# Optimization experiments

Measured on AMD Instinct MI355X. Metric: run time of the kernel, lower is better.

Reference implementation:

```python
import jax, jax.numpy as jnp
import numpy as np

N_ROWS = 1048576   # total clips
D = 128            # embedding dim
N_SEG = 2048       # number of videos (segments)
SEG_LEN = N_ROWS // N_SEG


def setup_inputs() -> dict:
    key = jax.random.key(0)
    k1, k2 = jax.random.split(key)
    clip_remap = jax.random.normal(k1, (N_ROWS, D), dtype=jnp.float32)
    clip_emb = jax.random.normal(k2, (N_ROWS, D), dtype=jnp.float32)
    # ragged segment lengths; constant here, must sum to N_ROWS
    num_list = jnp.full((N_SEG,), SEG_LEN, dtype=jnp.int32)
    return {"clip_remap": clip_remap, "clip_emb": clip_emb, "num_list": num_list}


def reference(clip_remap, clip_emb, num_list):
    n = clip_remap.shape[0]
    diff = clip_remap - clip_emb                       # [N, D]
    score_sub = jnp.sqrt(jnp.sum(diff * diff, axis=1))  # [N] per-row L2 distance
    # segment id per row from ragged lengths (static total length -> jit ok)
    seg_ids = jnp.repeat(jnp.arange(num_list.shape[0]), num_list,
                         total_repeat_length=n)        # [N]
    denom = num_list[seg_ids].astype(score_sub.dtype)  # [N] segment length per row
    return jnp.sum(score_sub / denom)                  # scalar loss
```

## Files before the change

### kernel.cpp

```cpp
#include <hip/hip_runtime.h>
#include <math.h>

typedef float v4f __attribute__((ext_vector_type(4)));

__global__ __launch_bounds__(256) void prep_kernel(const int* __restrict__ num_list,
                                                   int n_seg,
                                                   float* __restrict__ out,
                                                   int* __restrict__ seg_start) {
    __shared__ int s_sum[256];
    const int tid = threadIdx.x;
    const int C  = (n_seg + 255) >> 8;
    const int lo = tid * C;
    const int hi = (lo + C < n_seg) ? (lo + C) : n_seg;

    int sum = 0;
    for (int i = lo; i < hi; ++i) sum += num_list[i];
    s_sum[tid] = sum;
    __syncthreads();

    for (int off = 1; off < 256; off <<= 1) {
        int v   = s_sum[tid];
        int add = (tid >= off) ? s_sum[tid - off] : 0;
        __syncthreads();
        s_sum[tid] = v + add;
        __syncthreads();
    }

    int excl = (tid == 0) ? 0 : s_sum[tid - 1];
    for (int i = lo; i < hi; ++i) {
        seg_start[i] = excl;
        excl += num_list[i];
    }
    if (tid == 0) out[0] = 0.0f;
}

__global__ __launch_bounds__(256) void euclid_loss_kernel(
    const float* __restrict__ remap,
    const float* __restrict__ emb,
    const int*   __restrict__ num_list,
    const int*   __restrict__ seg_start_arr,
    float*       __restrict__ out)
{
    const int seg  = blockIdx.x;
    const int tid  = threadIdx.x;
    const int wid  = tid >> 6;
    const int lane = tid & 63;
    const int sub  = lane >> 5;
    const int l32  = lane & 31;

    const int seg_start = seg_start_arr[seg];
    const int seg_len   = num_list[seg];

    const v4f* __restrict__ pa = (const v4f*)remap;
    const v4f* __restrict__ pb = (const v4f*)emb;

    float acc = 0.0f;
    int r = wid * 2 + sub;

    for (; r + 8 < seg_len; r += 16) {
        const long long row0 = (long long)(seg_start + r);
        const long long row1 = row0 + 8;
        const v4f a0 = __builtin_nontemporal_load(pa + row0 * 32 + l32);
        const v4f b0 = __builtin_nontemporal_load(pb + row0 * 32 + l32);
        const v4f a1 = __builtin_nontemporal_load(pa + row1 * 32 + l32);
        const v4f b1 = __builtin_nontemporal_load(pb + row1 * 32 + l32);
        const v4f d0 = a0 - b0;
        const v4f d1 = a1 - b1;
        float s0 = d0[0]*d0[0] + d0[1]*d0[1] + d0[2]*d0[2] + d0[3]*d0[3];
        float s1 = d1[0]*d1[0] + d1[1]*d1[1] + d1[2]*d1[2] + d1[3]*d1[3];
        #pragma unroll
        for (int m = 1; m <= 16; m <<= 1) s0 += __shfl_xor(s0, m, 64);
        #pragma unroll
        for (int m = 1; m <= 16; m <<= 1) s1 += __shfl_xor(s1, m, 64);
        if (l32 == 0) acc += sqrtf(s0) + sqrtf(s1);
    }
    for (; r < seg_len; r += 8) {
        const long long row = (long long)(seg_start + r);
        const v4f a = __builtin_nontemporal_load(pa + row * 32 + l32);
        const v4f b = __builtin_nontemporal_load(pb + row * 32 + l32);
        const v4f d = a - b;
        float s = d[0]*d[0] + d[1]*d[1] + d[2]*d[2] + d[3]*d[3];
        #pragma unroll
        for (int m = 1; m <= 16; m <<= 1) s += __shfl_xor(s, m, 64);
        if (l32 == 0) acc += sqrtf(s);
    }

    #pragma unroll
    for (int off = 32; off >= 1; off >>= 1) acc += __shfl_down(acc, off, 64);
    __shared__ float s_acc[4];
    if (lane == 0) s_acc[wid] = acc;
    __syncthreads();
    if (tid == 0) {
        atomicAdd(out, (s_acc[0] + s_acc[1] + s_acc[2] + s_acc[3]) / (float)seg_len);
    }
}

extern "C" void kernel_launch(void* const* d_in, const int* in_sizes, int n_in,
                              void* d_out, int out_size, void* d_ws, size_t ws_size,
                              hipStream_t stream) {
    const float* remap    = (const float*)d_in[0];
    const float* emb      = (const float*)d_in[1];
    const int*   num_list = (const int*)d_in[2];
    float*       out      = (float*)d_out;
    int*         seg_start = (int*)d_ws;

    const int n_seg = in_sizes[2];

    prep_kernel<<<1, 256, 0, stream>>>(num_list, n_seg, out, seg_start);
    euclid_loss_kernel<<<n_seg, 256, 0, stream>>>(remap, emb, num_list, seg_start, out);
}
```

Before: 176.9 us.

## Compute segment offsets per block, unroll row loop, replace atomics with final reduce

Drops the single-block prefix-scan kernel: each block now sums num_list over the preceding segments itself to get its start row. Per-segment results are written to workspace and summed by a small final reduce kernel instead of atomically added. This gives a deterministic sum and removes the serial scan ahead of the main kernel. The main loop is unrolled to four rows per half-wave to keep more loads in flight. The cost is redundant prefix reads, which grow with the segment index, and an extra launch after the main kernel.

After: 166.5 us. -5.9%, faster.

```diff
diff --git a/kernel.cpp b/kernel.cpp
--- a/kernel.cpp
+++ b/kernel.cpp
@@ -3,43 +3,11 @@
 
 typedef float v4f __attribute__((ext_vector_type(4)));
 
-__global__ __launch_bounds__(256) void prep_kernel(const int* __restrict__ num_list,
-                                                   int n_seg,
-                                                   float* __restrict__ out,
-                                                   int* __restrict__ seg_start) {
-    __shared__ int s_sum[256];
-    const int tid = threadIdx.x;
-    const int C  = (n_seg + 255) >> 8;
-    const int lo = tid * C;
-    const int hi = (lo + C < n_seg) ? (lo + C) : n_seg;
-
-    int sum = 0;
-    for (int i = lo; i < hi; ++i) sum += num_list[i];
-    s_sum[tid] = sum;
-    __syncthreads();
-
-    for (int off = 1; off < 256; off <<= 1) {
-        int v   = s_sum[tid];
-        int add = (tid >= off) ? s_sum[tid - off] : 0;
-        __syncthreads();
-        s_sum[tid] = v + add;
-        __syncthreads();
-    }
-
-    int excl = (tid == 0) ? 0 : s_sum[tid - 1];
-    for (int i = lo; i < hi; ++i) {
-        seg_start[i] = excl;
-        excl += num_list[i];
-    }
-    if (tid == 0) out[0] = 0.0f;
-}
-
 __global__ __launch_bounds__(256) void euclid_loss_kernel(
     const float* __restrict__ remap,
     const float* __restrict__ emb,
     const int*   __restrict__ num_list,
-    const int*   __restrict__ seg_start_arr,
-    float*       __restrict__ out)
+    float*       __restrict__ ws)
 {
     const int seg  = blockIdx.x;
     const int tid  = threadIdx.x;
@@ -48,7 +16,19 @@
     const int sub  = lane >> 5;
     const int l32  = lane & 31;
 
-    const int seg_start = seg_start_arr[seg];
+    __shared__ int   s_red[4];
+    __shared__ int   s_start;
+    __shared__ float s_acc[4];
+
+    int partial = 0;
+    for (int i = tid; i < seg; i += 256) partial += num_list[i];
+    #pragma unroll
+    for (int off = 32; off >= 1; off >>= 1) partial += __shfl_down(partial, off, 64);
+    if (lane == 0) s_red[wid] = partial;
+    __syncthreads();
+    if (tid == 0) s_start = s_red[0] + s_red[1] + s_red[2] + s_red[3];
+    __syncthreads();
+    const int seg_start = s_start;
     const int seg_len   = num_list[seg];
 
     const v4f* __restrict__ pa = (const v4f*)remap;
@@ -57,22 +37,32 @@
     float acc = 0.0f;
     int r = wid * 2 + sub;
 
-    for (; r + 8 < seg_len; r += 16) {
+    for (; r + 24 < seg_len; r += 32) {
         const long long row0 = (long long)(seg_start + r);
-        const long long row1 = row0 + 8;
-        const v4f a0 = __builtin_nontemporal_load(pa + row0 * 32 + l32);
-        const v4f b0 = __builtin_nontemporal_load(pb + row0 * 32 + l32);
-        const v4f a1 = __builtin_nontemporal_load(pa + row1 * 32 + l32);
-        const v4f b1 = __builtin_nontemporal_load(pb + row1 * 32 + l32);
+        const v4f a0 = __builtin_nontemporal_load(pa + (row0     ) * 32 + l32);
+        const v4f b0 = __builtin_nontemporal_load(pb + (row0     ) * 32 + l32);
+        const v4f a1 = __builtin_nontemporal_load(pa + (row0 +  8) * 32 + l32);
+        const v4f b1 = __builtin_nontemporal_load(pb + (row0 +  8) * 32 + l32);
+        const v4f a2 = __builtin_nontemporal_load(pa + (row0 + 16) * 32 + l32);
+        const v4f b2 = __builtin_nontemporal_load(pb + (row0 + 16) * 32 + l32);
+        const v4f a3 = __builtin_nontemporal_load(pa + (row0 + 24) * 32 + l32);
+        const v4f b3 = __builtin_nontemporal_load(pb + (row0 + 24) * 32 + l32);
         const v4f d0 = a0 - b0;
         const v4f d1 = a1 - b1;
+        const v4f d2 = a2 - b2;
+        const v4f d3 = a3 - b3;
         float s0 = d0[0]*d0[0] + d0[1]*d0[1] + d0[2]*d0[2] + d0[3]*d0[3];
         float s1 = d1[0]*d1[0] + d1[1]*d1[1] + d1[2]*d1[2] + d1[3]*d1[3];
+        float s2 = d2[0]*d2[0] + d2[1]*d2[1] + d2[2]*d2[2] + d2[3]*d2[3];
+        float s3 = d3[0]*d3[0] + d3[1]*d3[1] + d3[2]*d3[2] + d3[3]*d3[3];
         #pragma unroll
-        for (int m = 1; m <= 16; m <<= 1) s0 += __shfl_xor(s0, m, 64);
-        #pragma unroll
-        for (int m = 1; m <= 16; m <<= 1) s1 += __shfl_xor(s1, m, 64);
-        if (l32 == 0) acc += sqrtf(s0) + sqrtf(s1);
+        for (int m = 1; m <= 16; m <<= 1) {
+            s0 += __shfl_xor(s0, m, 64);
+            s1 += __shfl_xor(s1, m, 64);
+            s2 += __shfl_xor(s2, m, 64);
+            s3 += __shfl_xor(s3, m, 64);
+        }
+        if (l32 == 0) acc += sqrtf(s0) + sqrtf(s1) + sqrtf(s2) + sqrtf(s3);
     }
     for (; r < seg_len; r += 8) {
         const long long row = (long long)(seg_start + r);
@@ -87,12 +77,28 @@
 
     #pragma unroll
     for (int off = 32; off >= 1; off >>= 1) acc += __shfl_down(acc, off, 64);
-    __shared__ float s_acc[4];
     if (lane == 0) s_acc[wid] = acc;
     __syncthreads();
     if (tid == 0) {
-        atomicAdd(out, (s_acc[0] + s_acc[1] + s_acc[2] + s_acc[3]) / (float)seg_len);
+        ws[seg] = (s_acc[0] + s_acc[1] + s_acc[2] + s_acc[3]) / (float)seg_len;
     }
+}
+
+__global__ __launch_bounds__(256) void final_reduce_kernel(
+    const float* __restrict__ ws, int n_seg, float* __restrict__ out)
+{
+    const int tid  = threadIdx.x;
+    const int wid  = tid >> 6;
+    const int lane = tid & 63;
+    __shared__ float s_acc[4];
+
+    float acc = 0.0f;
+    for (int i = tid; i < n_seg; i += 256) acc += ws[i];
+    #pragma unroll
+    for (int off = 32; off >= 1; off >>= 1) acc += __shfl_down(acc, off, 64);
+    if (lane == 0) s_acc[wid] = acc;
+    __syncthreads();
+    if (tid == 0) out[0] = s_acc[0] + s_acc[1] + s_acc[2] + s_acc[3];
 }
 
 extern "C" void kernel_launch(void* const* d_in, const int* in_sizes, int n_in,
@@ -102,10 +108,10 @@
     const float* emb      = (const float*)d_in[1];
     const int*   num_list = (const int*)d_in[2];
     float*       out      = (float*)d_out;
-    int*         seg_start = (int*)d_ws;
+    float*       ws       = (float*)d_ws;
 
     const int n_seg = in_sizes[2];
 
-    prep_kernel<<<1, 256, 0, stream>>>(num_list, n_seg, out, seg_start);
-    euclid_loss_kernel<<<n_seg, 256, 0, stream>>>(remap, emb, num_list, seg_start, out);
+    euclid_loss_kernel<<<n_seg, 256, 0, stream>>>(remap, emb, num_list, ws);
+    final_reduce_kernel<<<1, 256, 0, stream>>>(ws, n_seg, out);
 }
```
